# Optimization experiments

Hardware: AMD Instinct MI355X
Metric: run time of the kernel (lower is better)

## Reference

```python
import jax, jax.numpy as jnp
import numpy as np

N_NODES = 100000
N_EDGES = 300000
N_GRAPHS = 128
NODE_VOCAB = 200
NODE_DIM = 128
EDGE_VOCAB = 8
EDGE_DIM = 64
K_LAYERS = 3


def setup_inputs() -> dict:
    key = jax.random.key(0)
    ks = iter(jax.random.split(key, 40))
    f = lambda shape: jax.random.normal(next(ks), shape, dtype=jnp.float32)
    s = lambda shape: f(shape) * 0.05
    inp = {}
    inp["x_s"] = f((N_NODES, NODE_VOCAB))
    inp["x_t"] = f((N_NODES, NODE_VOCAB))
    inp["edge_attr_s"] = f((2 * N_EDGES, EDGE_VOCAB))
    inp["edge_attr_t"] = f((2 * N_EDGES, EDGE_VOCAB))
    inp["edge_index_s"] = jax.random.randint(next(ks), (2, N_EDGES), 0, N_NODES)
    inp["edge_index_t"] = jax.random.randint(next(ks), (2, N_EDGES), 0, N_NODES)
    inp["x_s_batch"] = jnp.sort(jax.random.randint(next(ks), (N_NODES,), 0, N_GRAPHS))
    inp["x_t_batch"] = jnp.sort(jax.random.randint(next(ks), (N_NODES,), 0, N_GRAPHS))
    inp["y"] = jax.random.randint(next(ks), (N_GRAPHS,), 0, 2)
    cat = 2 * NODE_DIM + EDGE_DIM  # 320: [x_src, edge_attr, x_dst]
    inp["node_emb"] = s((NODE_VOCAB, NODE_DIM))
    inp["edge_emb"] = s((EDGE_VOCAB, EDGE_DIM))
    inp["W_in_0"] = s((K_LAYERS, cat, EDGE_DIM))
    inp["W_in_1"] = s((K_LAYERS, EDGE_DIM, 1))
    inp["W_out_0"] = s((K_LAYERS, cat, EDGE_DIM))
    inp["W_out_1"] = s((K_LAYERS, EDGE_DIM, 1))
    inp["Wg_in"] = s((K_LAYERS, NODE_DIM, NODE_DIM))
    inp["bg_in"] = jnp.zeros((K_LAYERS, NODE_DIM), jnp.float32)
    inp["Wg_out"] = s((K_LAYERS, NODE_DIM, NODE_DIM))
    inp["bg_out"] = jnp.zeros((K_LAYERS, NODE_DIM), jnp.float32)
    inp["cls_W0"] = s((2 * NODE_DIM, NODE_DIM))
    inp["cls_b0"] = jnp.zeros((NODE_DIM,), jnp.float32)
    inp["cls_W1"] = s((NODE_DIM, 2))
    inp["cls_b1"] = jnp.zeros((2,), jnp.float32)
    return inp


def _dag_embed(x, e, row, col, W_in_0, W_in_1, W_out_0, W_out_1, Wg_in, bg_in, Wg_out, bg_out):
    N = x.shape[0]
    E = row.shape[0]
    for k in range(W_in_0.shape[0]):
        e_in, e_out = e[:E], e[E:]  # chunk(edge_attr_x, 2, dim=0)
        info_in = jnp.concatenate([x[row], e_in, x[col]], axis=1)   # [E, 2D+Ce]
        info_out = jnp.concatenate([x[col], e_out, x[row]], axis=1)
        e_in = info_in @ W_in_0[k]
        e_out = info_out @ W_out_0[k]
        w_in = jax.nn.sigmoid(e_in @ W_in_1[k]).ravel()   # [E]
        w_out = jax.nn.sigmoid(e_out @ W_out_1[k]).ravel()
        # embedding_in: flow source->target (x_j = x[row], aggregate at col)
        xi = x @ Wg_in[k]
        x_in = jax.ops.segment_sum(w_in[:, None] * xi[row], col, num_segments=N) + bg_in[k]
        # embedding_out: flow target->source (x_j = x[col], aggregate at row)
        xo = x @ Wg_out[k]
        x_out = jax.ops.segment_sum(w_out[:, None] * xo[col], row, num_segments=N) + bg_out[k]
        x = x + x_in + x_out
        e = jnp.concatenate([e_in, e_out], axis=0)
    return x


def _mean_pool(x, batch, num_graphs):
    sums = jax.ops.segment_sum(x, batch, num_segments=num_graphs)
    cnt = jax.ops.segment_sum(jnp.ones((x.shape[0], 1), x.dtype), batch, num_segments=num_graphs)
    return sums / jnp.maximum(cnt, 1.0)


def reference(x_s, x_t, edge_attr_s, edge_attr_t, edge_index_s, edge_index_t,
              x_s_batch, x_t_batch, y, node_emb, edge_emb,
              W_in_0, W_in_1, W_out_0, W_out_1, Wg_in, bg_in, Wg_out, bg_out,
              cls_W0, cls_b0, cls_W1, cls_b1):
    # Initialization: argmax -> embedding lookup
    h_s = node_emb[jnp.argmax(x_s, axis=1)]
    h_t = node_emb[jnp.argmax(x_t, axis=1)]
    he_s = edge_emb[jnp.argmax(edge_attr_s, axis=1)]
    he_t = edge_emb[jnp.argmax(edge_attr_t, axis=1)]
    h_s = _dag_embed(h_s, he_s, edge_index_s[0], edge_index_s[1],
                     W_in_0, W_in_1, W_out_0, W_out_1, Wg_in, bg_in, Wg_out, bg_out)
    h_t = _dag_embed(h_t, he_t, edge_index_t[0], edge_index_t[1],
                     W_in_0, W_in_1, W_out_0, W_out_1, Wg_in, bg_in, Wg_out, bg_out)
    g_s = _mean_pool(h_s, x_s_batch, N_GRAPHS)
    g_t = _mean_pool(h_t, x_t_batch, N_GRAPHS)
    h = jax.nn.relu(jnp.concatenate([g_s, g_t], axis=1) @ cls_W0 + cls_b0)
    logits = h @ cls_W1 + cls_b1
    logp = jax.nn.log_softmax(logits, axis=1)
    loss = -jnp.mean(jnp.take_along_axis(logp, y[:, None], axis=1))
    return loss
```

## Files before the change

### kernel.cpp

```cpp
#include <hip/hip_runtime.h>
#include <hip/hip_bf16.h>

#define N_NODES 100000
#define N_EDGES 300000
#define N_GRAPHS 128
#define NODE_VOCAB 200
#define NODE_DIM 128
#define EDGE_DIM 64
#define K_LAYERS 3

#define SCAN_CHUNK 2048
#define SCAN_NBLK ((N_NODES + SCAN_CHUNK - 1) / SCAN_CHUNK)

typedef unsigned short ushort_t;
typedef __attribute__((ext_vector_type(8))) __bf16 bf16x8;
typedef __attribute__((ext_vector_type(4))) float f32x4;

__device__ inline ushort_t f2bf(float f) {
    unsigned int u = __float_as_uint(f);
    unsigned int r = (u + 0x7fff + ((u >> 16) & 1)) >> 16;
    return (ushort_t)r;
}
__device__ inline float bf2f(ushort_t u) {
    return __uint_as_float(((unsigned int)u) << 16);
}
__device__ inline float bflo(unsigned int u) { return __uint_as_float(u << 16); }
__device__ inline float bfhi(unsigned int u) { return __uint_as_float(u & 0xffff0000u); }

#define MASK_J0 0x15151515u
#define MASK_J1 0x28282828u
#define MASK_J2 0x40404040u

__device__ ushort_t g_hb[2][(size_t)N_NODES * NODE_DIM];
__device__ ushort_t g_XWx_b[(size_t)N_NODES * 256];
__device__ ushort_t g_WcatT[K_LAYERS][256 * 128];
__device__ ushort_t g_QT[K_LAYERS][32][128];
__device__ float g_scal[(size_t)N_NODES * 32];
__device__ float g_bias[8][6];
__device__ int  g_evoc[2 * N_EDGES];
__device__ float g_gsum[2][N_GRAPHS * NODE_DIM];
__device__ float g_cnt[2][N_GRAPHS];
__device__ float g_H[N_GRAPHS * NODE_DIM];
__device__ int  g_deg_in[N_NODES];
__device__ int  g_deg_out[N_NODES];
__device__ int  g_off_in[N_NODES + 1];
__device__ int  g_off_out[N_NODES + 1];
__device__ int  g_cur_in[N_NODES];
__device__ int  g_cur_out[N_NODES];
__device__ int2 g_lst_in[N_EDGES];
__device__ int2 g_lst_out[N_EDGES];
__device__ int  g_bsum[2][SCAN_NBLK];
__device__ int  g_boff[2][SCAN_NBLK];

__global__ void node_embed_kernel(const float* __restrict__ x, const float* __restrict__ emb,
                                  int N) {
    int wave = threadIdx.x >> 6;
    int lane = threadIdx.x & 63;
    int n = blockIdx.x * 4 + wave;
    if (n >= N) return;
    const float* xr = x + (size_t)n * NODE_VOCAB;
    float v = xr[lane];
    int idx = lane;
    float nv = xr[lane + 64];
    if (nv > v) { v = nv; idx = lane + 64; }
    nv = xr[lane + 128];
    if (nv > v) { v = nv; idx = lane + 128; }
    if (lane < NODE_VOCAB - 192) {
        nv = xr[lane + 192];
        if (nv > v) { v = nv; idx = lane + 192; }
    }
    #pragma unroll
    for (int off = 32; off; off >>= 1) {
        float ov = __shfl_xor(v, off);
        int oi = __shfl_xor(idx, off);
        if (ov > v || (ov == v && oi < idx)) { v = ov; idx = oi; }
    }
    const float* er = emb + (size_t)idx * NODE_DIM;
    g_hb[0][(size_t)n * NODE_DIM + lane] = f2bf(er[lane]);
    g_hb[0][(size_t)n * NODE_DIM + 64 + lane] = f2bf(er[64 + lane]);
}

__global__ void edge_voc_kernel(const float* __restrict__ ea, int M) {
    long idx = (long)blockIdx.x * 256 + threadIdx.x;
    if (idx >= M) return;
    const float* ar = ea + idx * 8;
    float4 v0 = *(const float4*)ar;
    float4 v1 = *(const float4*)(ar + 4);
    float vals[8] = {v0.x, v0.y, v0.z, v0.w, v1.x, v1.y, v1.z, v1.w};
    int best = 0;
    float bv = vals[0];
    #pragma unroll
    for (int i = 1; i < 8; ++i)
        if (vals[i] > bv) { bv = vals[i]; best = i; }
    g_evoc[idx] = best;
}

__global__ void zero_qt_kernel() {
    int i = blockIdx.x * 256 + threadIdx.x;
    if (i < K_LAYERS * 32 * 128) ((ushort_t*)g_QT)[i] = 0;
}

__global__ void setup_gates_kernel(const float* __restrict__ Wi0, const float* __restrict__ Wi1,
                                   const float* __restrict__ Wo0, const float* __restrict__ Wo1,
                                   const float* __restrict__ eemb) {
    int b = blockIdx.x;
    int D = b / 3, k = b % 3;
    int t = threadIdx.x;
    const float* W0 = D ? Wo0 : Wi0;
    const float* W1 = D ? Wo1 : Wi1;
    __shared__ float u[64], un[64];
    if (t < 64) u[t] = W1[k * 64 + t];
    __syncthreads();
    int offk = (k == 0) ? 0 : (k == 1 ? 2 : 4);
    for (int j = k; j >= 0; --j) {
        const float* Wj = W0 + (size_t)j * 320 * 64;
        float qa = 0.f, qc = 0.f;
        for (int m = 0; m < 64; ++m) {
            float um = u[m];
            qa += Wj[t * 64 + m] * um;
            qc += Wj[(192 + t) * 64 + m] * um;
        }
        g_QT[j][(D ? 8 : 0) + offk + j][t] = f2bf(qa);
        g_QT[j][(D ? 24 : 16) + offk + j][t] = f2bf(qc);
        float s = 0.f;
        if (t < 64) {
            for (int m = 0; m < 64; ++m) s += Wj[(128 + t) * 64 + m] * u[m];
        }
        __syncthreads();
        if (t < 64) un[t] = s;
        __syncthreads();
        if (t < 64) u[t] = un[t];
        __syncthreads();
    }
    if (t < 8) {
        float s = 0.f;
        for (int m = 0; m < 64; ++m) s += eemb[t * 64 + m] * u[m];
        g_bias[t][D * 3 + k] = s;
    }
}

__global__ void csr_zero_kernel() {
    int i = blockIdx.x * 256 + threadIdx.x;
    if (i < N_NODES) { g_deg_in[i] = 0; g_deg_out[i] = 0; }
}

__global__ void csr_count_kernel(const int* __restrict__ row, const int* __restrict__ col,
                                 int E) {
    int e = blockIdx.x * 256 + threadIdx.x;
    if (e >= E) return;
    atomicAdd(&g_deg_in[col[e]], 1);
    atomicAdd(&g_deg_out[row[e]], 1);
}

__global__ void csr_bsum_kernel() {
    int which = blockIdx.y;
    const int* deg = which ? g_deg_out : g_deg_in;
    int b = blockIdx.x;
    int t = threadIdx.x;
    int base = b * SCAN_CHUNK;
    int s = 0;
    #pragma unroll
    for (int i = 0; i < SCAN_CHUNK / 256; ++i) {
        int idx = base + i * 256 + t;
        if (idx < N_NODES) s += deg[idx];
    }
    __shared__ int red[256];
    red[t] = s;
    __syncthreads();
    for (int d = 128; d; d >>= 1) {
        if (t < d) red[t] += red[t + d];
        __syncthreads();
    }
    if (t == 0) g_bsum[which][b] = red[0];
}

__global__ void csr_bscan_kernel() {
    int which = blockIdx.x;
    int t = threadIdx.x;
    int v = (t < SCAN_NBLK) ? g_bsum[which][t] : 0;
    int orig = v;
    #pragma unroll
    for (int d = 1; d < 64; d <<= 1) {
        int u = __shfl_up(v, d, 64);
        if (t >= d) v += u;
    }
    if (t < SCAN_NBLK) g_boff[which][t] = v - orig;
}

__global__ void csr_off_kernel(int total) {
    int which = blockIdx.y;
    const int* deg = which ? g_deg_out : g_deg_in;
    int* off = which ? g_off_out : g_off_in;
    int* cur = which ? g_cur_out : g_cur_in;
    int b = blockIdx.x;
    int t = threadIdx.x;
    const int per = SCAN_CHUNK / 256;
    int lo = b * SCAN_CHUNK + t * per;
    int d8[per];
    int s = 0;
    #pragma unroll
    for (int i = 0; i < per; ++i) {
        int idx = lo + i;
        d8[i] = (idx < N_NODES) ? deg[idx] : 0;
        s += d8[i];
    }
    __shared__ int part[256];
    part[t] = s;
    __syncthreads();
    for (int d = 1; d < 256; d <<= 1) {
        int add = (t >= d) ? part[t - d] : 0;
        __syncthreads();
        part[t] += add;
        __syncthreads();
    }
    int run = g_boff[which][b] + part[t] - s;
    #pragma unroll
    for (int i = 0; i < per; ++i) {
        int idx = lo + i;
        if (idx < N_NODES) {
            off[idx] = run;
            cur[idx] = run;
            run += d8[i];
        }
    }
    if (b == 0 && t == 0) off[N_NODES] = total;
}

__global__ void csr_fill_kernel(const int* __restrict__ row, const int* __restrict__ col,
                                int E) {
    int e = blockIdx.x * 256 + threadIdx.x;
    if (e >= E) return;
    int r = row[e], c = col[e];
    int p = atomicAdd(&g_cur_in[c], 1);
    g_lst_in[p] = make_int2(r, g_evoc[e]);
    int q = atomicAdd(&g_cur_out[r], 1);
    g_lst_out[q] = make_int2(c, g_evoc[E + e]);
}

__global__ void assemble_wcat_all(const float* __restrict__ Wgi, const float* __restrict__ Wgo) {
    int idx = blockIdx.x * 256 + threadIdx.x;
    if (idx >= K_LAYERS * 32768) return;
    int k = idx >> 15;
    int rem = idx & 32767;
    int n = rem >> 7;
    int kd = rem & 127;
    float v = (n < 128) ? Wgi[(size_t)k * 16384 + kd * 128 + n]
                        : Wgo[(size_t)k * 16384 + kd * 128 + (n - 128)];
    g_WcatT[k][n * 128 + kd] = f2bf(v);
}

__global__ __launch_bounds__(320) void gemm_xw_mfma(int cur, int layer, unsigned int mask,
                                                    int M) {
    const ushort_t* __restrict__ hb = g_hb[cur];
    int m0 = blockIdx.x * 64;
    int t = threadIdx.x;
    int wave = t >> 6, lane = t & 63;
    __shared__ ushort_t As[64 * 128];

    for (int idx = t; idx < 1024; idx += 320) {
        int m = idx >> 4, c = idx & 15;
        int gm = m0 + m;
        uint4 v = make_uint4(0u, 0u, 0u, 0u);
        if (gm < M) v = *(const uint4*)(hb + (size_t)gm * 128 + c * 8);
        *(uint4*)&As[m * 128 + ((c * 8) ^ ((m & 7) << 3))] = v;
    }
    __syncthreads();

    int lr = lane & 15, lk = lane >> 4;

    if (wave < 4) {
        int nbase = wave * 64;
        f32x4 acc[4][4];
        #pragma unroll
        for (int i = 0; i < 4; ++i)
            #pragma unroll
            for (int j = 0; j < 4; ++j)
                acc[i][j] = (f32x4){0.f, 0.f, 0.f, 0.f};

        const ushort_t* Bbase = &g_WcatT[layer][0] + (size_t)nbase * 128;
        #pragma unroll
        for (int ks = 0; ks < 4; ++ks) {
            bf16x8 a[4], b[4];
            int ke = ks * 32 + lk * 8;
            #pragma unroll
            for (int mt = 0; mt < 4; ++mt) {
                int row = mt * 16 + lr;
                a[mt] = *(const bf16x8*)&As[row * 128 + (ke ^ ((row & 7) << 3))];
            }
            #pragma unroll
            for (int nt = 0; nt < 4; ++nt) {
                b[nt] = *(const bf16x8*)(Bbase + (size_t)(nt * 16 + lr) * 128 + ke);
            }
            #pragma unroll
            for (int nt = 0; nt < 4; ++nt)
                #pragma unroll
                for (int mt = 0; mt < 4; ++mt)
                    acc[nt][mt] = __builtin_amdgcn_mfma_f32_16x16x32_bf16(b[nt], a[mt], acc[nt][mt], 0, 0, 0);
        }

        #pragma unroll
        for (int mt = 0; mt < 4; ++mt) {
            int gm = m0 + mt * 16 + lr;
            if (gm >= M) continue;
            #pragma unroll
            for (int nt = 0; nt < 4; ++nt) {
                int n0 = nbase + nt * 16 + lk * 4;
                f32x4 av = acc[nt][mt];
                uint2 pk;
                pk.x = ((unsigned int)f2bf(av[1]) << 16) | (unsigned int)f2bf(av[0]);
                pk.y = ((unsigned int)f2bf(av[3]) << 16) | (unsigned int)f2bf(av[2]);
                *(uint2*)&g_XWx_b[(size_t)gm * 256 + n0] = pk;
            }
        }
    } else {
        const ushort_t* QT = &g_QT[layer][0][0];
        f32x4 acc[2][4];
        #pragma unroll
        for (int i = 0; i < 2; ++i)
            #pragma unroll
            for (int j = 0; j < 4; ++j)
                acc[i][j] = (f32x4){0.f, 0.f, 0.f, 0.f};

        #pragma unroll
        for (int ks = 0; ks < 4; ++ks) {
            bf16x8 a[4], b[2];
            int ke = ks * 32 + lk * 8;
            #pragma unroll
            for (int mt = 0; mt < 4; ++mt) {
                int row = mt * 16 + lr;
                a[mt] = *(const bf16x8*)&As[row * 128 + (ke ^ ((row & 7) << 3))];
            }
            #pragma unroll
            for (int nt = 0; nt < 2; ++nt)
                b[nt] = *(const bf16x8*)&QT[(nt * 16 + lr) * 128 + ke];
            #pragma unroll
            for (int nt = 0; nt < 2; ++nt)
                #pragma unroll
                for (int mt = 0; mt < 4; ++mt)
                    acc[nt][mt] = __builtin_amdgcn_mfma_f32_16x16x32_bf16(b[nt], a[mt], acc[nt][mt], 0, 0, 0);
        }

        #pragma unroll
        for (int mt = 0; mt < 4; ++mt) {
            int gm = m0 + mt * 16 + lr;
            if (gm >= M) continue;
            #pragma unroll
            for (int nt = 0; nt < 2; ++nt) {
                #pragma unroll
                for (int r = 0; r < 4; ++r) {
                    int colc = nt * 16 + lk * 4 + r;
                    if ((mask >> colc) & 1u)
                        g_scal[(size_t)gm * 32 + colc] = acc[nt][mt][r];
                }
            }
        }
    }
}

__global__ __launch_bounds__(256) void aggregate_kernel(int cur, int k,
                                                        const float* __restrict__ bgi,
                                                        const float* __restrict__ bgo, int N) {
    int tid = threadIdx.x;
    int wv = tid >> 6;
    int lane = tid & 63;
    int grp = lane >> 4, li = lane & 15;
    int n = blockIdx.x * 16 + wv * 4 + grp;
    bool valid = n < N;

    int pin0 = 0, din = 0, pout0 = 0, dout = 0;
    float cin = 0.f, cout = 0.f;
    if (valid) {
        pin0 = g_off_in[n];  din = g_off_in[n + 1] - pin0;
        pout0 = g_off_out[n]; dout = g_off_out[n + 1] - pout0;
        const float* srow = g_scal + (size_t)n * 32;
        if (k == 0) {
            cin = srow[16]; cout = srow[24];
        } else if (k == 1) {
            cin = srow[18] + srow[19]; cout = srow[26] + srow[27];
        } else {
            cin = srow[20] + srow[21] + srow[22];
            cout = srow[28] + srow[29] + srow[30];
        }
    }
    int tot = din + dout;

    float acc[8];
    {
        float4 b1 = *(const float4*)(bgi + li * 8);
        float4 b2 = *(const float4*)(bgi + li * 8 + 4);
        float4 c1 = *(const float4*)(bgo + li * 8);
        float4 c2 = *(const float4*)(bgo + li * 8 + 4);
        uint4 xv = make_uint4(0u, 0u, 0u, 0u);
        if (valid) xv = *(const uint4*)(g_hb[cur] + (size_t)n * 128 + li * 8);
        acc[0] = bflo(xv.x) + b1.x + c1.x;
        acc[1] = bfhi(xv.x) + b1.y + c1.y;
        acc[2] = bflo(xv.y) + b1.z + c1.z;
        acc[3] = bfhi(xv.y) + b1.w + c1.w;
        acc[4] = bflo(xv.z) + b2.x + c2.x;
        acc[5] = bfhi(xv.z) + b2.y + c2.y;
        acc[6] = bflo(xv.w) + b2.z + c2.z;
        acc[7] = bfhi(xv.w) + b2.w + c2.w;
    }

    for (int base = 0; base < tot; base += 16) {
        int cnt = min(16, tot - base);
        float gate = 0.f;
        int sv = 0;
        if (li < cnt) {
            int q = base + li;
            int2 se;
            int dir;
            if (q < din) { se = g_lst_in[pin0 + q]; dir = 0; }
            else         { se = g_lst_out[pout0 + q - din]; dir = 1; }
            const float* arow = g_scal + (size_t)se.x * 32 + dir * 8;
            float asum;
            if (k == 0) asum = arow[0];
            else if (k == 1) asum = arow[2] + arow[3];
            else asum = arow[4] + arow[5] + arow[6];
            float s = g_bias[se.y][dir * 3 + k] + asum + (dir ? cout : cin);
            gate = 1.0f / (1.0f + __expf(-s));
            sv = se.x * 2 + dir;
        }
        for (int e = 0; e < cnt; ++e) {
            float wvv = __shfl(gate, grp * 16 + e);
            int s2 = __shfl(sv, grp * 16 + e);
            uint4 pv = *(const uint4*)(g_XWx_b + (size_t)(s2 >> 1) * 256 + (s2 & 1) * 128 + li * 8);
            acc[0] += wvv * bflo(pv.x);
            acc[1] += wvv * bfhi(pv.x);
            acc[2] += wvv * bflo(pv.y);
            acc[3] += wvv * bfhi(pv.y);
            acc[4] += wvv * bflo(pv.z);
            acc[5] += wvv * bfhi(pv.z);
            acc[6] += wvv * bflo(pv.w);
            acc[7] += wvv * bfhi(pv.w);
        }
    }

    if (valid) {
        uint4 pk;
        pk.x = ((unsigned int)f2bf(acc[1]) << 16) | (unsigned int)f2bf(acc[0]);
        pk.y = ((unsigned int)f2bf(acc[3]) << 16) | (unsigned int)f2bf(acc[2]);
        pk.z = ((unsigned int)f2bf(acc[5]) << 16) | (unsigned int)f2bf(acc[4]);
        pk.w = ((unsigned int)f2bf(acc[7]) << 16) | (unsigned int)f2bf(acc[6]);
        *(uint4*)(g_hb[cur ^ 1] + (size_t)n * 128 + li * 8) = pk;
    }
}

__global__ void pool_kernel(int fin, int side, const int* __restrict__ batch, int N) {
    const ushort_t* x = g_hb[fin];
    float* gsum = g_gsum[side];
    int n0 = blockIdx.x * 128;
    int d = threadIdx.x;
    if (n0 >= N) return;
    int nend = min(n0 + 128, N);
    float acc = 0.f;
    int curg = batch[n0];
    for (int n = n0; n < nend; ++n) {
        int g = batch[n];
        if (g != curg) {
            atomicAdd(&gsum[curg * 128 + d], acc);
            acc = 0.f;
            curg = g;
        }
        acc += bf2f(x[(size_t)n * 128 + d]);
    }
    atomicAdd(&gsum[curg * 128 + d], acc);
}

__global__ void count_kernel(int side, const int* __restrict__ batch, int N) {
    int g = threadIdx.x;
    int lo = 0, hi = N;
    while (lo < hi) { int mid = (lo + hi) >> 1; if (batch[mid] < g) lo = mid + 1; else hi = mid; }
    int a = lo;
    lo = 0; hi = N;
    while (lo < hi) { int mid = (lo + hi) >> 1; if (batch[mid] < g + 1) lo = mid + 1; else hi = mid; }
    g_cnt[side][g] = (float)(lo - a);
}

__global__ void zero_gsum_kernel() {
    int i = blockIdx.x * 256 + threadIdx.x;
    if (i < 2 * N_GRAPHS * NODE_DIM) ((float*)g_gsum)[i] = 0.f;
}

__global__ void hidden_kernel(const float* __restrict__ W0, const float* __restrict__ b0) {
    int g = blockIdx.x;
    int j = threadIdx.x;
    float inv_s = 1.0f / fmaxf(g_cnt[0][g], 1.0f);
    float inv_t = 1.0f / fmaxf(g_cnt[1][g], 1.0f);
    float acc = b0[j];
    for (int k = 0; k < 128; ++k) acc += g_gsum[0][g * 128 + k] * inv_s * W0[k * 128 + j];
    for (int k = 0; k < 128; ++k) acc += g_gsum[1][g * 128 + k] * inv_t * W0[(128 + k) * 128 + j];
    g_H[g * 128 + j] = fmaxf(acc, 0.f);
}

__global__ void loss_kernel(const float* __restrict__ W1, const float* __restrict__ b1,
                            const int* __restrict__ y, float* __restrict__ out) {
    int g = threadIdx.x;
    float l0 = b1[0], l1 = b1[1];
    for (int j = 0; j < 128; ++j) {
        float hv = g_H[g * 128 + j];
        l0 += hv * W1[j * 2 + 0];
        l1 += hv * W1[j * 2 + 1];
    }
    float m = fmaxf(l0, l1);
    float lse = m + logf(expf(l0 - m) + expf(l1 - m));
    float ly = (y[g] == 0) ? l0 : l1;
    float c = -(ly - lse) * (1.0f / (float)N_GRAPHS);
    __shared__ float red[128];
    red[g] = c;
    __syncthreads();
    for (int s = 64; s; s >>= 1) {
        if (g < s) red[g] += red[g + s];
        __syncthreads();
    }
    if (g == 0) out[0] = red[0];
}

extern "C" void kernel_launch(void* const* d_in, const int* in_sizes, int n_in,
                              void* d_out, int out_size, void* d_ws, size_t ws_size,
                              hipStream_t stream) {
    const float* x_s      = (const float*)d_in[0];
    const float* x_t      = (const float*)d_in[1];
    const float* ea_s     = (const float*)d_in[2];
    const float* ea_t     = (const float*)d_in[3];
    const int*   ei_s     = (const int*)d_in[4];
    const int*   ei_t     = (const int*)d_in[5];
    const int*   batch_s  = (const int*)d_in[6];
    const int*   batch_t  = (const int*)d_in[7];
    const int*   y        = (const int*)d_in[8];
    const float* node_emb = (const float*)d_in[9];
    const float* edge_emb = (const float*)d_in[10];
    const float* W_in_0   = (const float*)d_in[11];
    const float* W_in_1   = (const float*)d_in[12];
    const float* W_out_0  = (const float*)d_in[13];
    const float* W_out_1  = (const float*)d_in[14];
    const float* Wg_in    = (const float*)d_in[15];
    const float* bg_in    = (const float*)d_in[16];
    const float* Wg_out   = (const float*)d_in[17];
    const float* bg_out   = (const float*)d_in[18];
    const float* cls_W0   = (const float*)d_in[19];
    const float* cls_b0   = (const float*)d_in[20];
    const float* cls_W1   = (const float*)d_in[21];
    const float* cls_b1   = (const float*)d_in[22];

    const int N = N_NODES, E = N_EDGES;
    static const unsigned int MASKS[3] = {MASK_J0, MASK_J1, MASK_J2};

    zero_gsum_kernel<<<(2 * N_GRAPHS * NODE_DIM + 255) / 256, 256, 0, stream>>>();
    zero_qt_kernel<<<(K_LAYERS * 32 * 128 + 255) / 256, 256, 0, stream>>>();
    setup_gates_kernel<<<6, 128, 0, stream>>>(W_in_0, W_in_1, W_out_0, W_out_1, edge_emb);
    assemble_wcat_all<<<(K_LAYERS * 32768 + 255) / 256, 256, 0, stream>>>(Wg_in, Wg_out);

    for (int side = 0; side < 2; ++side) {
        const float* xin   = side ? x_t : x_s;
        const float* eain  = side ? ea_t : ea_s;
        const int*   ei    = side ? ei_t : ei_s;
        const int*   batch = side ? batch_t : batch_s;
        const int* row = ei;
        const int* col = ei + E;

        node_embed_kernel<<<(N + 3) / 4, 256, 0, stream>>>(xin, node_emb, N);
        edge_voc_kernel<<<(2 * E + 255) / 256, 256, 0, stream>>>(eain, 2 * E);

        csr_zero_kernel<<<(N + 255) / 256, 256, 0, stream>>>();
        csr_count_kernel<<<(E + 255) / 256, 256, 0, stream>>>(row, col, E);
        csr_bsum_kernel<<<dim3(SCAN_NBLK, 2), 256, 0, stream>>>();
        csr_bscan_kernel<<<2, 64, 0, stream>>>();
        csr_off_kernel<<<dim3(SCAN_NBLK, 2), 256, 0, stream>>>(E);
        csr_fill_kernel<<<(E + 255) / 256, 256, 0, stream>>>(row, col, E);

        int cur = 0;
        for (int k = 0; k < K_LAYERS; ++k) {
            gemm_xw_mfma<<<(N + 63) / 64, 320, 0, stream>>>(cur, k, MASKS[k], N);
            aggregate_kernel<<<(N + 15) / 16, 256, 0, stream>>>(
                cur, k, bg_in + (size_t)k * 128, bg_out + (size_t)k * 128, N);
            cur ^= 1;
        }
        pool_kernel<<<(N + 127) / 128, 128, 0, stream>>>(cur, side, batch, N);
        count_kernel<<<1, 128, 0, stream>>>(side, batch, N);
    }

    hidden_kernel<<<128, 128, 0, stream>>>(cls_W0, cls_b0);
    loss_kernel<<<1, 128, 0, stream>>>(cls_W1, cls_b1, y, (float*)d_out);
}
```

Baseline: 899.1 us.

## Batch both graph sides and interleave GEMM of one side with aggregation of other

New measurement: 1.077 ms. +19.8%, slower.

```diff
diff --git a/kernel.cpp b/kernel.cpp
--- a/kernel.cpp
+++ b/kernel.cpp
@@ -11,6 +11,8 @@
 
 #define SCAN_CHUNK 2048
 #define SCAN_NBLK ((N_NODES + SCAN_CHUNK - 1) / SCAN_CHUNK)
+#define GEMM_NB ((N_NODES + 63) / 64)
+#define AGG_NB ((N_NODES + 19) / 20)
 
 typedef unsigned short ushort_t;
 typedef __attribute__((ext_vector_type(8))) __bf16 bf16x8;
@@ -31,72 +33,26 @@
 #define MASK_J1 0x28282828u
 #define MASK_J2 0x40404040u
 
-__device__ ushort_t g_hb[2][(size_t)N_NODES * NODE_DIM];
-__device__ ushort_t g_XWx_b[(size_t)N_NODES * 256];
+__device__ ushort_t g_hb[2][2][(size_t)N_NODES * NODE_DIM];
+__device__ ushort_t g_XWx_b[2][(size_t)N_NODES * 256];
 __device__ ushort_t g_WcatT[K_LAYERS][256 * 128];
 __device__ ushort_t g_QT[K_LAYERS][32][128];
-__device__ float g_scal[(size_t)N_NODES * 32];
+__device__ float g_scal[2][(size_t)N_NODES * 32];
 __device__ float g_bias[8][6];
-__device__ int  g_evoc[2 * N_EDGES];
+__device__ int  g_evoc[2][2 * N_EDGES];
 __device__ float g_gsum[2][N_GRAPHS * NODE_DIM];
 __device__ float g_cnt[2][N_GRAPHS];
 __device__ float g_H[N_GRAPHS * NODE_DIM];
-__device__ int  g_deg_in[N_NODES];
-__device__ int  g_deg_out[N_NODES];
-__device__ int  g_off_in[N_NODES + 1];
-__device__ int  g_off_out[N_NODES + 1];
-__device__ int  g_cur_in[N_NODES];
-__device__ int  g_cur_out[N_NODES];
-__device__ int2 g_lst_in[N_EDGES];
-__device__ int2 g_lst_out[N_EDGES];
-__device__ int  g_bsum[2][SCAN_NBLK];
-__device__ int  g_boff[2][SCAN_NBLK];
-
-__global__ void node_embed_kernel(const float* __restrict__ x, const float* __restrict__ emb,
-                                  int N) {
-    int wave = threadIdx.x >> 6;
-    int lane = threadIdx.x & 63;
-    int n = blockIdx.x * 4 + wave;
-    if (n >= N) return;
-    const float* xr = x + (size_t)n * NODE_VOCAB;
-    float v = xr[lane];
-    int idx = lane;
-    float nv = xr[lane + 64];
-    if (nv > v) { v = nv; idx = lane + 64; }
-    nv = xr[lane + 128];
-    if (nv > v) { v = nv; idx = lane + 128; }
-    if (lane < NODE_VOCAB - 192) {
-        nv = xr[lane + 192];
-        if (nv > v) { v = nv; idx = lane + 192; }
-    }
-    #pragma unroll
-    for (int off = 32; off; off >>= 1) {
-        float ov = __shfl_xor(v, off);
-        int oi = __shfl_xor(idx, off);
-        if (ov > v || (ov == v && oi < idx)) { v = ov; idx = oi; }
-    }
-    const float* er = emb + (size_t)idx * NODE_DIM;
-    g_hb[0][(size_t)n * NODE_DIM + lane] = f2bf(er[lane]);
-    g_hb[0][(size_t)n * NODE_DIM + 64 + lane] = f2bf(er[64 + lane]);
-}
-
-__global__ void edge_voc_kernel(const float* __restrict__ ea, int M) {
-    long idx = (long)blockIdx.x * 256 + threadIdx.x;
-    if (idx >= M) return;
-    const float* ar = ea + idx * 8;
-    float4 v0 = *(const float4*)ar;
-    float4 v1 = *(const float4*)(ar + 4);
-    float vals[8] = {v0.x, v0.y, v0.z, v0.w, v1.x, v1.y, v1.z, v1.w};
-    int best = 0;
-    float bv = vals[0];
-    #pragma unroll
-    for (int i = 1; i < 8; ++i)
-        if (vals[i] > bv) { bv = vals[i]; best = i; }
-    g_evoc[idx] = best;
-}
-
-__global__ void zero_qt_kernel() {
+__device__ int  g_deg[2][2][N_NODES];
+__device__ int  g_off[2][2][N_NODES + 1];
+__device__ int  g_cur[2][2][N_NODES];
+__device__ int2 g_lst[2][2][N_EDGES];
+__device__ int  g_bsum[2][2][SCAN_NBLK];
+__device__ int  g_boff[2][2][SCAN_NBLK];
+
+__global__ void zero_misc_kernel() {
     int i = blockIdx.x * 256 + threadIdx.x;
+    if (i < 2 * N_GRAPHS * NODE_DIM) ((float*)g_gsum)[i] = 0.f;
     if (i < K_LAYERS * 32 * 128) ((ushort_t*)g_QT)[i] = 0;
 }
 
@@ -139,22 +95,84 @@
     }
 }
 
+__global__ void assemble_wcat_all(const float* __restrict__ Wgi, const float* __restrict__ Wgo) {
+    int idx = blockIdx.x * 256 + threadIdx.x;
+    if (idx >= K_LAYERS * 32768) return;
+    int k = idx >> 15;
+    int rem = idx & 32767;
+    int n = rem >> 7;
+    int kd = rem & 127;
+    float v = (n < 128) ? Wgi[(size_t)k * 16384 + kd * 128 + n]
+                        : Wgo[(size_t)k * 16384 + kd * 128 + (n - 128)];
+    g_WcatT[k][n * 128 + kd] = f2bf(v);
+}
+
+__global__ void node_embed_kernel(const float* __restrict__ x_s, const float* __restrict__ x_t,
+                                  const float* __restrict__ emb, int N) {
+    int side = blockIdx.y;
+    const float* x = side ? x_t : x_s;
+    int wave = threadIdx.x >> 6;
+    int lane = threadIdx.x & 63;
+    int n = blockIdx.x * 4 + wave;
+    if (n >= N) return;
+    const float* xr = x + (size_t)n * NODE_VOCAB;
+    float v = xr[lane];
+    int idx = lane;
+    float nv = xr[lane + 64];
+    if (nv > v) { v = nv; idx = lane + 64; }
+    nv = xr[lane + 128];
+    if (nv > v) { v = nv; idx = lane + 128; }
+    if (lane < NODE_VOCAB - 192) {
+        nv = xr[lane + 192];
+        if (nv > v) { v = nv; idx = lane + 192; }
+    }
+    #pragma unroll
+    for (int off = 32; off; off >>= 1) {
+        float ov = __shfl_xor(v, off);
+        int oi = __shfl_xor(idx, off);
+        if (ov > v || (ov == v && oi < idx)) { v = ov; idx = oi; }
+    }
+    const float* er = emb + (size_t)idx * NODE_DIM;
+    g_hb[side][0][(size_t)n * NODE_DIM + lane] = f2bf(er[lane]);
+    g_hb[side][0][(size_t)n * NODE_DIM + 64 + lane] = f2bf(er[64 + lane]);
+}
+
+__global__ void edge_voc_kernel(const float* __restrict__ ea_s, const float* __restrict__ ea_t,
+                                int M) {
+    int side = blockIdx.y;
+    const float* ea = side ? ea_t : ea_s;
+    long idx = (long)blockIdx.x * 256 + threadIdx.x;
+    if (idx >= M) return;
+    const float* ar = ea + idx * 8;
+    float4 v0 = *(const float4*)ar;
+    float4 v1 = *(const float4*)(ar + 4);
+    float vals[8] = {v0.x, v0.y, v0.z, v0.w, v1.x, v1.y, v1.z, v1.w};
+    int best = 0;
+    float bv = vals[0];
+    #pragma unroll
+    for (int i = 1; i < 8; ++i)
+        if (vals[i] > bv) { bv = vals[i]; best = i; }
+    g_evoc[side][idx] = best;
+}
+
 __global__ void csr_zero_kernel() {
     int i = blockIdx.x * 256 + threadIdx.x;
-    if (i < N_NODES) { g_deg_in[i] = 0; g_deg_out[i] = 0; }
-}
-
-__global__ void csr_count_kernel(const int* __restrict__ row, const int* __restrict__ col,
+    if (i < 4 * N_NODES) ((int*)g_deg)[i] = 0;
+}
+
+__global__ void csr_count_kernel(const int* __restrict__ ei_s, const int* __restrict__ ei_t,
                                  int E) {
+    int side = blockIdx.y;
+    const int* ei = side ? ei_t : ei_s;
     int e = blockIdx.x * 256 + threadIdx.x;
     if (e >= E) return;
-    atomicAdd(&g_deg_in[col[e]], 1);
-    atomicAdd(&g_deg_out[row[e]], 1);
+    atomicAdd(&g_deg[side][0][ei[E + e]], 1);
+    atomicAdd(&g_deg[side][1][ei[e]], 1);
 }
 
 __global__ void csr_bsum_kernel() {
-    int which = blockIdx.y;
-    const int* deg = which ? g_deg_out : g_deg_in;
+    int dir = blockIdx.y, side = blockIdx.z;
+    const int* deg = g_deg[side][dir];
     int b = blockIdx.x;
     int t = threadIdx.x;
     int base = b * SCAN_CHUNK;
@@ -171,27 +189,27 @@
         if (t < d) red[t] += red[t + d];
         __syncthreads();
     }
-    if (t == 0) g_bsum[which][b] = red[0];
+    if (t == 0) g_bsum[side][dir][b] = red[0];
 }
 
 __global__ void csr_bscan_kernel() {
-    int which = blockIdx.x;
+    int dir = blockIdx.x, side = blockIdx.y;
     int t = threadIdx.x;
-    int v = (t < SCAN_NBLK) ? g_bsum[which][t] : 0;
+    int v = (t < SCAN_NBLK) ? g_bsum[side][dir][t] : 0;
     int orig = v;
     #pragma unroll
     for (int d = 1; d < 64; d <<= 1) {
         int u = __shfl_up(v, d, 64);
         if (t >= d) v += u;
     }
-    if (t < SCAN_NBLK) g_boff[which][t] = v - orig;
+    if (t < SCAN_NBLK) g_boff[side][dir][t] = v - orig;
 }
 
 __global__ void csr_off_kernel(int total) {
-    int which = blockIdx.y;
-    const int* deg = which ? g_deg_out : g_deg_in;
-    int* off = which ? g_off_out : g_off_in;
-    int* cur = which ? g_cur_out : g_cur_in;
+    int dir = blockIdx.y, side = blockIdx.z;
+    const int* deg = g_deg[side][dir];
+    int* off = g_off[side][dir];
+    int* cur = g_cur[side][dir];
     int b = blockIdx.x;
     int t = threadIdx.x;
     const int per = SCAN_CHUNK / 256;
@@ -213,7 +231,7 @@
         part[t] += add;
         __syncthreads();
     }
-    int run = g_boff[which][b] + part[t] - s;
+    int run = g_boff[side][dir][b] + part[t] - s;
     #pragma unroll
     for (int i = 0; i < per; ++i) {
         int idx = lo + i;
@@ -226,36 +244,25 @@
     if (b == 0 && t == 0) off[N_NODES] = total;
 }
 
-__global__ void csr_fill_kernel(const int* __restrict__ row, const int* __restrict__ col,
+__global__ void csr_fill_kernel(const int* __restrict__ ei_s, const int* __restrict__ ei_t,
                                 int E) {
+    int side = blockIdx.y;
+    const int* ei = side ? ei_t : ei_s;
     int e = blockIdx.x * 256 + threadIdx.x;
     if (e >= E) return;
-    int r = row[e], c = col[e];
-    int p = atomicAdd(&g_cur_in[c], 1);
-    g_lst_in[p] = make_int2(r, g_evoc[e]);
-    int q = atomicAdd(&g_cur_out[r], 1);
-    g_lst_out[q] = make_int2(c, g_evoc[E + e]);
-}
-
-__global__ void assemble_wcat_all(const float* __restrict__ Wgi, const float* __restrict__ Wgo) {
-    int idx = blockIdx.x * 256 + threadIdx.x;
-    if (idx >= K_LAYERS * 32768) return;
-    int k = idx >> 15;
-    int rem = idx & 32767;
-    int n = rem >> 7;
-    int kd = rem & 127;
-    float v = (n < 128) ? Wgi[(size_t)k * 16384 + kd * 128 + n]
-                        : Wgo[(size_t)k * 16384 + kd * 128 + (n - 128)];
-    g_WcatT[k][n * 128 + kd] = f2bf(v);
-}
-
-__global__ __launch_bounds__(320) void gemm_xw_mfma(int cur, int layer, unsigned int mask,
-                                                    int M) {
-    const ushort_t* __restrict__ hb = g_hb[cur];
-    int m0 = blockIdx.x * 64;
+    int r = ei[e], c = ei[E + e];
+    int p = atomicAdd(&g_cur[side][0][c], 1);
+    g_lst[side][0][p] = make_int2(r, g_evoc[side][e]);
+    int q = atomicAdd(&g_cur[side][1][r], 1);
+    g_lst[side][1][q] = make_int2(c, g_evoc[side][E + e]);
+}
+
+__device__ __forceinline__ void gemm_body(int blk, int side, int layer, unsigned int mask,
+                                          ushort_t* As, int M) {
+    const ushort_t* __restrict__ hb = g_hb[side][layer & 1];
+    int m0 = blk * 64;
     int t = threadIdx.x;
     int wave = t >> 6, lane = t & 63;
-    __shared__ ushort_t As[64 * 128];
 
     for (int idx = t; idx < 1024; idx += 320) {
         int m = idx >> 4, c = idx & 15;
@@ -288,9 +295,8 @@
                 a[mt] = *(const bf16x8*)&As[row * 128 + (ke ^ ((row & 7) << 3))];
             }
             #pragma unroll
-            for (int nt = 0; nt < 4; ++nt) {
+            for (int nt = 0; nt < 4; ++nt)
                 b[nt] = *(const bf16x8*)(Bbase + (size_t)(nt * 16 + lr) * 128 + ke);
-            }
             #pragma unroll
             for (int nt = 0; nt < 4; ++nt)
                 #pragma unroll
@@ -298,6 +304,7 @@
                     acc[nt][mt] = __builtin_amdgcn_mfma_f32_16x16x32_bf16(b[nt], a[mt], acc[nt][mt], 0, 0, 0);
         }
 
+        ushort_t* XW = g_XWx_b[side];
         #pragma unroll
         for (int mt = 0; mt < 4; ++mt) {
             int gm = m0 + mt * 16 + lr;
@@ -309,7 +316,7 @@
                 uint2 pk;
                 pk.x = ((unsigned int)f2bf(av[1]) << 16) | (unsigned int)f2bf(av[0]);
                 pk.y = ((unsigned int)f2bf(av[3]) << 16) | (unsigned int)f2bf(av[2]);
-                *(uint2*)&g_XWx_b[(size_t)gm * 256 + n0] = pk;
+                *(uint2*)&XW[(size_t)gm * 256 + n0] = pk;
             }
         }
     } else {
@@ -340,6 +347,7 @@
                     acc[nt][mt] = __builtin_amdgcn_mfma_f32_16x16x32_bf16(b[nt], a[mt], acc[nt][mt], 0, 0, 0);
         }
 
+        float* sc = g_scal[side];
         #pragma unroll
         for (int mt = 0; mt < 4; ++mt) {
             int gm = m0 + mt * 16 + lr;
@@ -350,29 +358,32 @@
                 for (int r = 0; r < 4; ++r) {
                     int colc = nt * 16 + lk * 4 + r;
                     if ((mask >> colc) & 1u)
-                        g_scal[(size_t)gm * 32 + colc] = acc[nt][mt][r];
+                        sc[(size_t)gm * 32 + colc] = acc[nt][mt][r];
                 }
             }
         }
     }
 }
 
-__global__ __launch_bounds__(256) void aggregate_kernel(int cur, int k,
-                                                        const float* __restrict__ bgi,
-                                                        const float* __restrict__ bgo, int N) {
-    int tid = threadIdx.x;
-    int wv = tid >> 6;
-    int lane = tid & 63;
+__device__ __forceinline__ void agg_body(int blk, int side, int k,
+                                         const float* __restrict__ bgi,
+                                         const float* __restrict__ bgo, int N) {
+    int t = threadIdx.x;
+    int wv = t >> 6;
+    int lane = t & 63;
     int grp = lane >> 4, li = lane & 15;
-    int n = blockIdx.x * 16 + wv * 4 + grp;
+    int n = blk * 20 + wv * 4 + grp;
     bool valid = n < N;
+    int cur = k & 1;
+    const float* scal = g_scal[side];
+    const ushort_t* XW = g_XWx_b[side];
 
     int pin0 = 0, din = 0, pout0 = 0, dout = 0;
     float cin = 0.f, cout = 0.f;
     if (valid) {
-        pin0 = g_off_in[n];  din = g_off_in[n + 1] - pin0;
-        pout0 = g_off_out[n]; dout = g_off_out[n + 1] - pout0;
-        const float* srow = g_scal + (size_t)n * 32;
+        pin0 = g_off[side][0][n];  din = g_off[side][0][n + 1] - pin0;
+        pout0 = g_off[side][1][n]; dout = g_off[side][1][n + 1] - pout0;
+        const float* srow = scal + (size_t)n * 32;
         if (k == 0) {
             cin = srow[16]; cout = srow[24];
         } else if (k == 1) {
@@ -391,7 +402,7 @@
         float4 c1 = *(const float4*)(bgo + li * 8);
         float4 c2 = *(const float4*)(bgo + li * 8 + 4);
         uint4 xv = make_uint4(0u, 0u, 0u, 0u);
-        if (valid) xv = *(const uint4*)(g_hb[cur] + (size_t)n * 128 + li * 8);
+        if (valid) xv = *(const uint4*)(g_hb[side][cur] + (size_t)n * 128 + li * 8);
         acc[0] = bflo(xv.x) + b1.x + c1.x;
         acc[1] = bfhi(xv.x) + b1.y + c1.y;
         acc[2] = bflo(xv.y) + b1.z + c1.z;
@@ -410,9 +421,9 @@
             int q = base + li;
             int2 se;
             int dir;
-            if (q < din) { se = g_lst_in[pin0 + q]; dir = 0; }
-            else         { se = g_lst_out[pout0 + q - din]; dir = 1; }
-            const float* arow = g_scal + (size_t)se.x * 32 + dir * 8;
+            if (q < din) { se = g_lst[side][0][pin0 + q]; dir = 0; }
+            else         { se = g_lst[side][1][pout0 + q - din]; dir = 1; }
+            const float* arow = scal + (size_t)se.x * 32 + dir * 8;
             float asum;
             if (k == 0) asum = arow[0];
             else if (k == 1) asum = arow[2] + arow[3];
@@ -421,18 +432,35 @@
             gate = 1.0f / (1.0f + __expf(-s));
             sv = se.x * 2 + dir;
         }
-        for (int e = 0; e < cnt; ++e) {
-            float wvv = __shfl(gate, grp * 16 + e);
-            int s2 = __shfl(sv, grp * 16 + e);
-            uint4 pv = *(const uint4*)(g_XWx_b + (size_t)(s2 >> 1) * 256 + (s2 & 1) * 128 + li * 8);
-            acc[0] += wvv * bflo(pv.x);
-            acc[1] += wvv * bfhi(pv.x);
-            acc[2] += wvv * bflo(pv.y);
-            acc[3] += wvv * bfhi(pv.y);
-            acc[4] += wvv * bflo(pv.z);
-            acc[5] += wvv * bfhi(pv.z);
-            acc[6] += wvv * bflo(pv.w);
-            acc[7] += wvv * bfhi(pv.w);
+        int e = 0;
+        for (; e + 2 <= cnt; e += 2) {
+            float w0 = __shfl(gate, grp * 16 + e);
+            int a0 = __shfl(sv, grp * 16 + e);
+            float w1 = __shfl(gate, grp * 16 + e + 1);
+            int a1 = __shfl(sv, grp * 16 + e + 1);
+            uint4 p0 = *(const uint4*)(XW + (size_t)(a0 >> 1) * 256 + (a0 & 1) * 128 + li * 8);
+            uint4 p1 = *(const uint4*)(XW + (size_t)(a1 >> 1) * 256 + (a1 & 1) * 128 + li * 8);
+            acc[0] += w0 * bflo(p0.x) + w1 * bflo(p1.x);
+            acc[1] += w0 * bfhi(p0.x) + w1 * bfhi(p1.x);
+            acc[2] += w0 * bflo(p0.y) + w1 * bflo(p1.y);
+            acc[3] += w0 * bfhi(p0.y) + w1 * bfhi(p1.y);
+            acc[4] += w0 * bflo(p0.z) + w1 * bflo(p1.z);
+            acc[5] += w0 * bfhi(p0.z) + w1 * bfhi(p1.z);
+            acc[6] += w0 * bflo(p0.w) + w1 * bflo(p1.w);
+            acc[7] += w0 * bfhi(p0.w) + w1 * bfhi(p1.w);
+        }
+        if (e < cnt) {
+            float w0 = __shfl(gate, grp * 16 + e);
+            int a0 = __shfl(sv, grp * 16 + e);
+            uint4 p0 = *(const uint4*)(XW + (size_t)(a0 >> 1) * 256 + (a0 & 1) * 128 + li * 8);
+            acc[0] += w0 * bflo(p0.x);
+            acc[1] += w0 * bfhi(p0.x);
+            acc[2] += w0 * bflo(p0.y);
+            acc[3] += w0 * bfhi(p0.y);
+            acc[4] += w0 * bflo(p0.z);
+            acc[5] += w0 * bfhi(p0.z);
+            acc[6] += w0 * bflo(p0.w);
+            acc[7] += w0 * bfhi(p0.w);
         }
     }
 
@@ -442,12 +470,32 @@
         pk.y = ((unsigned int)f2bf(acc[3]) << 16) | (unsigned int)f2bf(acc[2]);
         pk.z = ((unsigned int)f2bf(acc[5]) << 16) | (unsigned int)f2bf(acc[4]);
         pk.w = ((unsigned int)f2bf(acc[7]) << 16) | (unsigned int)f2bf(acc[6]);
-        *(uint4*)(g_hb[cur ^ 1] + (size_t)n * 128 + li * 8) = pk;
-    }
-}
-
-__global__ void pool_kernel(int fin, int side, const int* __restrict__ batch, int N) {
-    const ushort_t* x = g_hb[fin];
+        *(uint4*)(g_hb[side][cur ^ 1] + (size_t)n * 128 + li * 8) = pk;
+    }
+}
+
+__global__ __launch_bounds__(320) void fused_step(const float* __restrict__ bgi,
+                                                  const float* __restrict__ bgo,
+                                                  int gemm_side, int gemm_layer,
+                                                  unsigned int mask,
+                                                  int agg_side, int agg_layer,
+                                                  int gemm_nb, int total, int N) {
+    __shared__ ushort_t As[64 * 128];
+    int bid = blockIdx.x;
+    int g_before = (int)(((long)bid * gemm_nb) / total);
+    int g_next = (int)(((long)(bid + 1) * gemm_nb) / total);
+    if (g_next > g_before) {
+        gemm_body(g_before, gemm_side, gemm_layer, mask, As, N);
+    } else {
+        agg_body(bid - g_before, agg_side, agg_layer, bgi, bgo, N);
+    }
+}
+
+__global__ void pool_kernel(const int* __restrict__ batch_s, const int* __restrict__ batch_t,
+                            int N) {
+    int side = blockIdx.y;
+    const int* batch = side ? batch_t : batch_s;
+    const ushort_t* x = g_hb[side][K_LAYERS & 1];
     float* gsum = g_gsum[side];
     int n0 = blockIdx.x * 128;
     int d = threadIdx.x;
@@ -467,7 +515,10 @@
     atomicAdd(&gsum[curg * 128 + d], acc);
 }
 
-__global__ void count_kernel(int side, const int* __restrict__ batch, int N) {
+__global__ void count_kernel(const int* __restrict__ batch_s, const int* __restrict__ batch_t,
+                             int N) {
+    int side = blockIdx.x;
+    const int* batch = side ? batch_t : batch_s;
     int g = threadIdx.x;
     int lo = 0, hi = N;
     while (lo < hi) { int mid = (lo + hi) >> 1; if (batch[mid] < g) lo = mid + 1; else hi = mid; }
@@ -475,11 +526,6 @@
     lo = 0; hi = N;
     while (lo < hi) { int mid = (lo + hi) >> 1; if (batch[mid] < g + 1) lo = mid + 1; else hi = mid; }
     g_cnt[side][g] = (float)(lo - a);
-}
-
-__global__ void zero_gsum_kernel() {
-    int i = blockIdx.x * 256 + threadIdx.x;
-    if (i < 2 * N_GRAPHS * NODE_DIM) ((float*)g_gsum)[i] = 0.f;
 }
 
 __global__ void hidden_kernel(const float* __restrict__ W0, const float* __restrict__ b0) {
@@ -546,39 +592,36 @@
     const int N = N_NODES, E = N_EDGES;
     static const unsigned int MASKS[3] = {MASK_J0, MASK_J1, MASK_J2};
 
-    zero_gsum_kernel<<<(2 * N_GRAPHS * NODE_DIM + 255) / 256, 256, 0, stream>>>();
-    zero_qt_kernel<<<(K_LAYERS * 32 * 128 + 255) / 256, 256, 0, stream>>>();
+    zero_misc_kernel<<<(2 * N_GRAPHS * NODE_DIM + 255) / 256, 256, 0, stream>>>();
     setup_gates_kernel<<<6, 128, 0, stream>>>(W_in_0, W_in_1, W_out_0, W_out_1, edge_emb);
     assemble_wcat_all<<<(K_LAYERS * 32768 + 255) / 256, 256, 0, stream>>>(Wg_in, Wg_out);
 
-    for (int side = 0; side < 2; ++side) {
-        const float* xin   = side ? x_t : x_s;
-        const float* eain  = side ? ea_t : ea_s;
-        const int*   ei    = side ? ei_t : ei_s;
-        const int*   batch = side ? batch_t : batch_s;
-        const int* row = ei;
-        const int* col = ei + E;
-
-        node_embed_kernel<<<(N + 3) / 4, 256, 0, stream>>>(xin, node_emb, N);
-        edge_voc_kernel<<<(2 * E + 255) / 256, 256, 0, stream>>>(eain, 2 * E);
-
-        csr_zero_kernel<<<(N + 255) / 256, 256, 0, stream>>>();
-        csr_count_kernel<<<(E + 255) / 256, 256, 0, stream>>>(row, col, E);
-        csr_bsum_kernel<<<dim3(SCAN_NBLK, 2), 256, 0, stream>>>();
-        csr_bscan_kernel<<<2, 64, 0, stream>>>();
-        csr_off_kernel<<<dim3(SCAN_NBLK, 2), 256, 0, stream>>>(E);
-        csr_fill_kernel<<<(E + 255) / 256, 256, 0, stream>>>(row, col, E);
-
-        int cur = 0;
-        for (int k = 0; k < K_LAYERS; ++k) {
-            gemm_xw_mfma<<<(N + 63) / 64, 320, 0, stream>>>(cur, k, MASKS[k], N);
-            aggregate_kernel<<<(N + 15) / 16, 256, 0, stream>>>(
-                cur, k, bg_in + (size_t)k * 128, bg_out + (size_t)k * 128, N);
-            cur ^= 1;
-        }
-        pool_kernel<<<(N + 127) / 128, 128, 0, stream>>>(cur, side, batch, N);
-        count_kernel<<<1, 128, 0, stream>>>(side, batch, N);
-    }
+    node_embed_kernel<<<dim3((N + 3) / 4, 2), 256, 0, stream>>>(x_s, x_t, node_emb, N);
+    edge_voc_kernel<<<dim3((2 * E + 255) / 256, 2), 256, 0, stream>>>(ea_s, ea_t, 2 * E);
+
+    csr_zero_kernel<<<(4 * N + 255) / 256, 256, 0, stream>>>();
+    csr_count_kernel<<<dim3((E + 255) / 256, 2), 256, 0, stream>>>(ei_s, ei_t, E);
+    csr_bsum_kernel<<<dim3(SCAN_NBLK, 2, 2), 256, 0, stream>>>();
+    csr_bscan_kernel<<<dim3(2, 2), 64, 0, stream>>>();
+    csr_off_kernel<<<dim3(SCAN_NBLK, 2, 2), 256, 0, stream>>>(E);
+    csr_fill_kernel<<<dim3((E + 255) / 256, 2), 256, 0, stream>>>(ei_s, ei_t, E);
+
+    const int FULL = GEMM_NB + AGG_NB;
+    fused_step<<<GEMM_NB, 320, 0, stream>>>(bg_in, bg_out, 0, 0, MASKS[0], -1, 0, GEMM_NB,
+                                            GEMM_NB, N);
+    fused_step<<<FULL, 320, 0, stream>>>(bg_in, bg_out, 1, 0, MASKS[0], 0, 0, GEMM_NB, FULL, N);
+    fused_step<<<FULL, 320, 0, stream>>>(bg_in, bg_out, 0, 1, MASKS[1], 1, 0, GEMM_NB, FULL, N);
+    fused_step<<<FULL, 320, 0, stream>>>(bg_in + 128, bg_out + 128, 1, 1, MASKS[1], 0, 1,
+                                         GEMM_NB, FULL, N);
+    fused_step<<<FULL, 320, 0, stream>>>(bg_in + 128, bg_out + 128, 0, 2, MASKS[2], 1, 1,
+                                         GEMM_NB, FULL, N);
+    fused_step<<<FULL, 320, 0, stream>>>(bg_in + 256, bg_out + 256, 1, 2, MASKS[2], 0, 2,
+                                         GEMM_NB, FULL, N);
+    fused_step<<<AGG_NB, 320, 0, stream>>>(bg_in + 256, bg_out + 256, 0, 0, 0u, 1, 2, 0,
+                                           AGG_NB, N);
+
+    pool_kernel<<<dim3((N + 127) / 128, 2), 128, 0, stream>>>(batch_s, batch_t, N);
+    count_kernel<<<2, 128, 0, stream>>>(batch_s, batch_t, N);
 
     hidden_kernel<<<128, 128, 0, stream>>>(cls_W0, cls_b0);
     loss_kernel<<<1, 128, 0, stream>>>(cls_W1, cls_b1, y, (float*)d_out);
```
